# Kernel optimization log

Measured on AMD Instinct MI355X. Metric: run time of the kernel, lower is better.

The kernel has to match this reference:

```python
import jax, jax.numpy as jnp
import numpy as np

L, E, TOP_K = 3, 8, 2
B, N, D, DS = 256, 1024, 512, 128

def setup_inputs() -> dict:
    key = jax.random.key(0)
    ks = jax.random.split(key, 10)
    s = 0.05  # weight init scale
    return {
        "token": jax.random.normal(ks[0], (B, 1, D), jnp.float32),
        "node_emb": jax.random.normal(ks[1], (B, N, D), jnp.float32),
        "states": jnp.zeros((L, E, B, DS), jnp.float32),
        "Wg": jax.random.normal(ks[2], (L, D, E), jnp.float32) * s,
        "bg": jnp.zeros((L, E), jnp.float32),
        "A": jax.random.normal(ks[3], (L, E, DS), jnp.float32),
        "Bin": jax.random.normal(ks[4], (L, E, D, DS), jnp.float32) * s,
        "Cout": jax.random.normal(ks[5], (L, E, DS, D), jnp.float32) * s,
        "Dsk": jax.random.normal(ks[6], (L, E, D), jnp.float32) * s,
        "Wq": jax.random.normal(ks[7], (D, D), jnp.float32) * s,
        "bq": jnp.zeros((D,), jnp.float32),
    }

def reference(token, node_emb, states, Wg, bg, A, Bin, Cout, Dsk, Wq, bq):
    # token: (B,1,D) -> h: (B,D)
    h = token[:, 0, :]
    lb_loss = jnp.float32(0.0)
    new_states = []
    for l in range(L):
        # --- MoE router: top-k softmax gating ---
        probs = jax.nn.softmax(h @ Wg[l] + bg[l])              # (B,E)
        topv, topi = jax.lax.top_k(probs, TOP_K)               # (B,k)
        gates_k = topv / jnp.sum(topv, axis=-1, keepdims=True)  # renormalized
        oh = jax.nn.one_hot(topi, E, dtype=probs.dtype)        # (B,k,E)
        gate_full = jnp.einsum('bk,bke->be', gates_k, oh)      # (B,E)
        sel = jnp.sum(oh, axis=1) > 0                          # (B,E) bool
        # --- state-space experts (computed densely for all experts) ---
        s = states[l]                                          # (E,B,DS)
        decay = jax.nn.sigmoid(A[l])[:, None, :]               # (E,1,DS)
        s_new = decay * s + jnp.einsum('bd,eds->ebs', h, Bin[l])   # (E,B,DS)
        y = jnp.einsum('ebs,esd->ebd', s_new, Cout[l]) + h[None] * Dsk[l][:, None, :]
        out = jnp.einsum('be,ebd->bd', gate_full, y)           # weighted combine
        # only routed experts advance their state
        keep = sel.T[:, :, None]                               # (E,B,1)
        new_states.append(jnp.where(keep, s_new, s))
        # load-balance loss: E * sum_e mean(probs_e) * mean(frac routed to e)
        lb_loss = lb_loss + E * jnp.sum(jnp.mean(probs, axis=0) * jnp.mean(sel.astype(probs.dtype), axis=0))
        h = h + out                                            # residual
    # --- query projection + logits over nodes ---
    q = h @ Wq + bq                                            # (B,D)
    logits = jnp.einsum('bd,bnd->bn', q, node_emb) / jnp.sqrt(jnp.float32(D))
    return logits, jnp.stack(new_states), lb_loss
```

## Files before the change

### kernel.cpp

```cpp
#include <hip/hip_runtime.h>
#include <math.h>

#define LNUM 3
#define ENUM 8
#define TOPK 2
#define BSZ 256
#define NSZ 1024
#define DSZ 512
#define SSZ 128

typedef float f32x4 __attribute__((ext_vector_type(4)));

__global__ __launch_bounds__(1024, 2) void fused_kernel(
    const float* __restrict__ token,
    const float* __restrict__ states,
    const float* __restrict__ Wg,
    const float* __restrict__ bg,
    const float* __restrict__ A,
    const float* __restrict__ Bin,
    const float* __restrict__ Cout,
    const float* __restrict__ Dsk,
    const float* __restrict__ Wq,
    const float* __restrict__ bq,
    float* __restrict__ out_states,
    float* __restrict__ acc,
    float* __restrict__ q_out)
{
    const int b = blockIdx.x;
    const int t = threadIdx.x;
    const int wave = t >> 6;
    const int lane = t & 63;

    __shared__ float h_s[DSZ];
    __shared__ float yacc_s[DSZ];
    __shared__ float snew_s[TOPK][SSZ];
    __shared__ float logit_s[ENUM];
    __shared__ f32x4 part4[1024];
    float* part = (float*)part4;

    if (t < DSZ) h_s[t] = token[b * DSZ + t];

    for (int l = 0; l < LNUM; ++l) {
        const float* Wg_l  = Wg  + (size_t)l * DSZ * ENUM;
        const float* bg_l  = bg  + (size_t)l * ENUM;
        const float* A_l   = A   + (size_t)l * ENUM * SSZ;
        const float* Bin_l = Bin + (size_t)l * ENUM * DSZ * SSZ;
        const float* Cou_l = Cout+ (size_t)l * ENUM * SSZ * DSZ;
        const float* Dsk_l = Dsk + (size_t)l * ENUM * DSZ;
        const float* st_l  = states     + (size_t)l * ENUM * BSZ * SSZ;
        float*       os_l  = out_states + (size_t)l * ENUM * BSZ * SSZ;

        __syncthreads();
        part4[t] = ((const f32x4*)Wg_l)[t];
        __syncthreads();

        if (wave < ENUM) {
            float p = 0.f;
            #pragma unroll
            for (int i = 0; i < 8; ++i) {
                const int d = lane + i * 64;
                p = fmaf(h_s[d], part[d * ENUM + wave], p);
            }
            for (int off = 32; off; off >>= 1) p += __shfl_down(p, off, 64);
            if (lane == 0) logit_s[wave] = p + bg_l[wave];
        }
        __syncthreads();

        float probs[ENUM];
        float mx = logit_s[0];
        for (int e = 1; e < ENUM; ++e) mx = fmaxf(mx, logit_s[e]);
        float ssum = 0.f;
        for (int e = 0; e < ENUM; ++e) { probs[e] = expf(logit_s[e] - mx); ssum += probs[e]; }
        const float sinv = 1.f / ssum;
        for (int e = 0; e < ENUM; ++e) probs[e] *= sinv;

        int i0 = 0;
        for (int e = 1; e < ENUM; ++e) if (probs[e] > probs[i0]) i0 = e;
        int i1 = -1;
        for (int e = 0; e < ENUM; ++e) {
            if (e == i0) continue;
            if (i1 < 0 || probs[e] > probs[i1]) i1 = e;
        }
        float g0 = probs[i0], g1 = probs[i1];
        const float ginv = 1.f / (g0 + g1);
        g0 *= ginv; g1 *= ginv;

        if (t < ENUM) {
            atomicAdd(&acc[(l * 2 + 0) * ENUM + t], probs[t]);
            atomicAdd(&acc[(l * 2 + 1) * ENUM + t], (t == i0 || t == i1) ? 1.0f : 0.0f);
        }

        #pragma unroll
        for (int k = 0; k < TOPK; ++k) {
            const int e = k ? i1 : i0;
            {
                const int c  = t >> 5;
                const int sq = t & 31;
                const float* Bp = Bin_l + (size_t)e * DSZ * SSZ + sq * 4;
                const int d0 = c * 16;
                f32x4 acc4 = {0.f, 0.f, 0.f, 0.f};
                #pragma unroll
                for (int d = 0; d < 16; ++d)
                    acc4 += *(const f32x4*)(Bp + (size_t)(d0 + d) * SSZ) * h_s[d0 + d];
                part4[c * 32 + sq] = acc4;
            }
            __syncthreads();
            if (t < SSZ) {
                float sum = 0.f;
                #pragma unroll
                for (int c = 0; c < 32; ++c) sum += part[c * 128 + t];
                const float a = A_l[e * SSZ + t];
                const float decay = 1.f / (1.f + expf(-a));
                snew_s[k][t] = decay * st_l[((size_t)e * BSZ + b) * SSZ + t] + sum;
            }
            __syncthreads();
        }

        {
            const int e = t >> 7, s = t & 127;
            float v;
            if (e == i0)      v = snew_s[0][s];
            else if (e == i1) v = snew_s[1][s];
            else              v = st_l[((size_t)e * BSZ + b) * SSZ + s];
            os_l[((size_t)e * BSZ + b) * SSZ + s] = v;
        }

        #pragma unroll
        for (int k = 0; k < TOPK; ++k) {
            const int e = k ? i1 : i0;
            const float g = k ? g1 : g0;
            {
                const int sc = t >> 7;
                const int dq = t & 127;
                const float* Cp = Cou_l + (size_t)e * SSZ * DSZ + dq * 4;
                const float* sp = snew_s[k];
                const int s0 = sc * 16;
                f32x4 acc4 = {0.f, 0.f, 0.f, 0.f};
                #pragma unroll
                for (int s = 0; s < 16; ++s)
                    acc4 += *(const f32x4*)(Cp + (size_t)(s0 + s) * DSZ) * sp[s0 + s];
                part4[sc * 128 + dq] = acc4;
            }
            __syncthreads();
            if (t < DSZ) {
                float yk = 0.f;
                #pragma unroll
                for (int sc = 0; sc < 8; ++sc) yk += part[sc * 512 + t];
                const float hd = h_s[t];
                yk = g * (yk + hd * Dsk_l[e * DSZ + t]);
                if (k == 0) yacc_s[t] = yk;
                else        h_s[t] = hd + yacc_s[t] + yk;
            }
            __syncthreads();
        }
    }

    {
        const int chunk = t >> 7;
        const int dquad = t & 127;
        const int dd0 = chunk * 64;
        f32x4 acc4 = {0.f, 0.f, 0.f, 0.f};
        #pragma unroll 8
        for (int i = 0; i < 64; ++i)
            acc4 += *(const f32x4*)(Wq + (size_t)(dd0 + i) * DSZ + dquad * 4) * h_s[dd0 + i];
        part4[chunk * 128 + dquad] = acc4;
    }
    __syncthreads();
    if (t < DSZ) {
        float qv = bq[t];
        #pragma unroll
        for (int c = 0; c < 8; ++c) qv += part[c * 512 + t];
        q_out[b * DSZ + t] = qv;
    }
}

__global__ __launch_bounds__(256) void logits_kernel(
    const float* __restrict__ q, const float* __restrict__ node_emb,
    float* __restrict__ logits,
    const float* __restrict__ acc, float* __restrict__ loss_out)
{
    const int b = blockIdx.y;
    const int wave = threadIdx.x >> 6;
    const int lane = threadIdx.x & 63;

    if (blockIdx.x == 0 && blockIdx.y == 0 && threadIdx.x == 0) {
        float lb = 0.f;
        for (int l = 0; l < LNUM; ++l)
            for (int e = 0; e < ENUM; ++e) {
                const float mp = acc[(l * 2 + 0) * ENUM + e] * (1.0f / BSZ);
                const float ms = acc[(l * 2 + 1) * ENUM + e] * (1.0f / BSZ);
                lb += (float)ENUM * mp * ms;
            }
        loss_out[0] = lb;
    }

    const f32x4* q4 = (const f32x4*)(q + b * DSZ);
    const f32x4 q0 = q4[lane];
    const f32x4 q1 = q4[lane + 64];
    const float scale = 0.04419417382415922f;

    const int n0 = blockIdx.x * 128 + wave * 32;
    for (int i = 0; i < 32; i += 2) {
        const f32x4* r0 = (const f32x4*)(node_emb + ((size_t)b * NSZ + n0 + i) * DSZ);
        const f32x4* r1 = (const f32x4*)(node_emb + ((size_t)b * NSZ + n0 + i + 1) * DSZ);
        const f32x4 a0 = __builtin_nontemporal_load(r0 + lane);
        const f32x4 a1 = __builtin_nontemporal_load(r0 + lane + 64);
        const f32x4 c0 = __builtin_nontemporal_load(r1 + lane);
        const f32x4 c1 = __builtin_nontemporal_load(r1 + lane + 64);
        float d0 = a0.x*q0.x + a0.y*q0.y + a0.z*q0.z + a0.w*q0.w
                 + a1.x*q1.x + a1.y*q1.y + a1.z*q1.z + a1.w*q1.w;
        float d1 = c0.x*q0.x + c0.y*q0.y + c0.z*q0.z + c0.w*q0.w
                 + c1.x*q1.x + c1.y*q1.y + c1.z*q1.z + c1.w*q1.w;
        #pragma unroll
        for (int off = 32; off; off >>= 1) {
            d0 += __shfl_down(d0, off, 64);
            d1 += __shfl_down(d1, off, 64);
        }
        if (lane == 0) {
            logits[b * NSZ + n0 + i]     = d0 * scale;
            logits[b * NSZ + n0 + i + 1] = d1 * scale;
        }
    }
}

extern "C" void kernel_launch(void* const* d_in, const int* in_sizes, int n_in,
                              void* d_out, int out_size, void* d_ws, size_t ws_size,
                              hipStream_t stream) {
    const float* token    = (const float*)d_in[0];
    const float* node_emb = (const float*)d_in[1];
    const float* states   = (const float*)d_in[2];
    const float* Wg       = (const float*)d_in[3];
    const float* bg       = (const float*)d_in[4];
    const float* A        = (const float*)d_in[5];
    const float* Bin      = (const float*)d_in[6];
    const float* Cout     = (const float*)d_in[7];
    const float* Dsk      = (const float*)d_in[8];
    const float* Wq       = (const float*)d_in[9];
    const float* bq       = (const float*)d_in[10];

    float* out_logits = (float*)d_out;
    float* out_states = out_logits + (size_t)BSZ * NSZ;
    float* out_loss   = out_states + (size_t)LNUM * ENUM * BSZ * SSZ;

    float* ws_q   = (float*)d_ws;
    float* ws_acc = ws_q + (size_t)BSZ * DSZ;

    (void)hipMemsetAsync(ws_acc, 0, sizeof(float) * LNUM * 16, stream);

    fused_kernel<<<BSZ, 1024, 0, stream>>>(
        token, states, Wg, bg, A, Bin, Cout, Dsk, Wq, bq,
        out_states, ws_acc, ws_q);

    dim3 lg(NSZ / 128, BSZ);
    logits_kernel<<<lg, 256, 0, stream>>>(ws_q, node_emb, out_logits, ws_acc, out_loss);
}
```

Baseline: 164.5 us.

## Fuse node logits computation into the per-batch fused kernel

Moves the q·node_emb logits dot products into the end of the main per-batch kernel, keeping q in shared memory instead of writing it to workspace and launching a separate logits kernel. The load-balance loss reduction moves to a tiny separate kernel. This removes a kernel launch and the q round trip through global memory. The risk is less parallelism for the bandwidth-heavy node_emb stream, which now runs on 256 large blocks instead of 2048 smaller ones.

```diff
diff --git a/kernel.cpp b/kernel.cpp
--- a/kernel.cpp
+++ b/kernel.cpp
@@ -11,8 +11,9 @@
 
 typedef float f32x4 __attribute__((ext_vector_type(4)));
 
-__global__ __launch_bounds__(1024, 2) void fused_kernel(
+__global__ __launch_bounds__(1024, 2) void mega_kernel(
     const float* __restrict__ token,
+    const float* __restrict__ node_emb,
     const float* __restrict__ states,
     const float* __restrict__ Wg,
     const float* __restrict__ bg,
@@ -22,9 +23,9 @@
     const float* __restrict__ Dsk,
     const float* __restrict__ Wq,
     const float* __restrict__ bq,
+    float* __restrict__ out_logits,
     float* __restrict__ out_states,
-    float* __restrict__ acc,
-    float* __restrict__ q_out)
+    float* __restrict__ acc)
 {
     const int b = blockIdx.x;
     const int t = threadIdx.x;
@@ -170,20 +171,42 @@
         float qv = bq[t];
         #pragma unroll
         for (int c = 0; c < 8; ++c) qv += part[c * 512 + t];
-        q_out[b * DSZ + t] = qv;
+        yacc_s[t] = qv;
+    }
+    __syncthreads();
+
+    {
+        const f32x4 q0 = ((const f32x4*)yacc_s)[lane];
+        const f32x4 q1 = ((const f32x4*)yacc_s)[lane + 64];
+        const float scale = 0.04419417382415922f;
+        const int n0 = wave * 64;
+        for (int i = 0; i < 64; i += 2) {
+            const f32x4* r0 = (const f32x4*)(node_emb + ((size_t)b * NSZ + n0 + i) * DSZ);
+            const f32x4* r1 = (const f32x4*)(node_emb + ((size_t)b * NSZ + n0 + i + 1) * DSZ);
+            const f32x4 a0 = __builtin_nontemporal_load(r0 + lane);
+            const f32x4 a1 = __builtin_nontemporal_load(r0 + lane + 64);
+            const f32x4 c0 = __builtin_nontemporal_load(r1 + lane);
+            const f32x4 c1 = __builtin_nontemporal_load(r1 + lane + 64);
+            float d0 = a0.x*q0.x + a0.y*q0.y + a0.z*q0.z + a0.w*q0.w
+                     + a1.x*q1.x + a1.y*q1.y + a1.z*q1.z + a1.w*q1.w;
+            float d1 = c0.x*q0.x + c0.y*q0.y + c0.z*q0.z + c0.w*q0.w
+                     + c1.x*q1.x + c1.y*q1.y + c1.z*q1.z + c1.w*q1.w;
+            #pragma unroll
+            for (int off = 32; off; off >>= 1) {
+                d0 += __shfl_down(d0, off, 64);
+                d1 += __shfl_down(d1, off, 64);
+            }
+            if (lane == 0) {
+                out_logits[b * NSZ + n0 + i]     = d0 * scale;
+                out_logits[b * NSZ + n0 + i + 1] = d1 * scale;
+            }
+        }
     }
 }
 
-__global__ __launch_bounds__(256) void logits_kernel(
-    const float* __restrict__ q, const float* __restrict__ node_emb,
-    float* __restrict__ logits,
-    const float* __restrict__ acc, float* __restrict__ loss_out)
+__global__ void loss_kernel(const float* __restrict__ acc, float* __restrict__ out)
 {
-    const int b = blockIdx.y;
-    const int wave = threadIdx.x >> 6;
-    const int lane = threadIdx.x & 63;
-
-    if (blockIdx.x == 0 && blockIdx.y == 0 && threadIdx.x == 0) {
+    if (threadIdx.x == 0) {
         float lb = 0.f;
         for (int l = 0; l < LNUM; ++l)
             for (int e = 0; e < ENUM; ++e) {
@@ -191,35 +214,7 @@
                 const float ms = acc[(l * 2 + 1) * ENUM + e] * (1.0f / BSZ);
                 lb += (float)ENUM * mp * ms;
             }
-        loss_out[0] = lb;
-    }
-
-    const f32x4* q4 = (const f32x4*)(q + b * DSZ);
-    const f32x4 q0 = q4[lane];
-    const f32x4 q1 = q4[lane + 64];
-    const float scale = 0.04419417382415922f;
-
-    const int n0 = blockIdx.x * 128 + wave * 32;
-    for (int i = 0; i < 32; i += 2) {
-        const f32x4* r0 = (const f32x4*)(node_emb + ((size_t)b * NSZ + n0 + i) * DSZ);
-        const f32x4* r1 = (const f32x4*)(node_emb + ((size_t)b * NSZ + n0 + i + 1) * DSZ);
-        const f32x4 a0 = __builtin_nontemporal_load(r0 + lane);
-        const f32x4 a1 = __builtin_nontemporal_load(r0 + lane + 64);
-        const f32x4 c0 = __builtin_nontemporal_load(r1 + lane);
-        const f32x4 c1 = __builtin_nontemporal_load(r1 + lane + 64);
-        float d0 = a0.x*q0.x + a0.y*q0.y + a0.z*q0.z + a0.w*q0.w
-                 + a1.x*q1.x + a1.y*q1.y + a1.z*q1.z + a1.w*q1.w;
-        float d1 = c0.x*q0.x + c0.y*q0.y + c0.z*q0.z + c0.w*q0.w
-                 + c1.x*q1.x + c1.y*q1.y + c1.z*q1.z + c1.w*q1.w;
-        #pragma unroll
-        for (int off = 32; off; off >>= 1) {
-            d0 += __shfl_down(d0, off, 64);
-            d1 += __shfl_down(d1, off, 64);
-        }
-        if (lane == 0) {
-            logits[b * NSZ + n0 + i]     = d0 * scale;
-            logits[b * NSZ + n0 + i + 1] = d1 * scale;
-        }
+        out[0] = lb;
     }
 }
 
@@ -242,15 +237,13 @@
     float* out_states = out_logits + (size_t)BSZ * NSZ;
     float* out_loss   = out_states + (size_t)LNUM * ENUM * BSZ * SSZ;
 
-    float* ws_q   = (float*)d_ws;
-    float* ws_acc = ws_q + (size_t)BSZ * DSZ;
+    float* ws_acc = (float*)d_ws;
 
     (void)hipMemsetAsync(ws_acc, 0, sizeof(float) * LNUM * 16, stream);
 
-    fused_kernel<<<BSZ, 1024, 0, stream>>>(
-        token, states, Wg, bg, A, Bin, Cout, Dsk, Wq, bq,
-        out_states, ws_acc, ws_q);
-
-    dim3 lg(NSZ / 128, BSZ);
-    logits_kernel<<<lg, 256, 0, stream>>>(ws_q, node_emb, out_logits, ws_acc, out_loss);
+    mega_kernel<<<BSZ, 1024, 0, stream>>>(
+        token, node_emb, states, Wg, bg, A, Bin, Cout, Dsk, Wq, bq,
+        out_logits, out_states, ws_acc);
+
+    loss_kernel<<<1, 64, 0, stream>>>(ws_acc, out_loss);
 }
```

Result: faster. 160.1 us (-2.6%).
